# Optimization experiments

Measured on AMD Instinct MI355X. Metric: run time of the kernel, lower is better.

The kernel has to match this reference:

```python
import jax, jax.numpy as jnp
import numpy as np

B, N, D = 8, 2048, 512
S = 4096  # max_swaps


def setup_inputs() -> dict:
    key = jax.random.key(0)
    ks = jax.random.split(key, 5)
    h = jax.random.normal(ks[0], (B, N, D), dtype=jnp.float32)
    indices = jax.random.randint(ks[1], (B, S, 4), 0, N, dtype=jnp.int64)
    # MLP params (Linear stores weight as (out,in) in torch; we keep (in,out) and matmul)
    W1 = jax.random.normal(ks[2], (4 * D, D), dtype=jnp.float32) * (1.0 / np.sqrt(4 * D))
    b1 = jnp.zeros((D,), dtype=jnp.float32)
    W2 = jax.random.normal(ks[3], (D, D // 2), dtype=jnp.float32) * (1.0 / np.sqrt(D))
    b2 = jnp.zeros((D // 2,), dtype=jnp.float32)
    W3 = jax.random.normal(ks[4], (D // 2, 1), dtype=jnp.float32) * (1.0 / np.sqrt(D // 2))
    b3 = jnp.zeros((1,), dtype=jnp.float32)
    return {"h": h, "indices": indices, "W1": W1, "b1": b1, "W2": W2, "b2": b2, "W3": W3, "b3": b3}


def reference(h, indices, W1, b1, W2, b2, W3, b3):
    # h: (B, N, D); indices: (B, S, 4) node ids per swap
    swap_emb = jnp.take_along_axis(h[:, None, :, :], indices[..., None].astype(jnp.int32),
                                   axis=2)  # broadcast-gather -> (B, S, 4, D)
    # equivalently: h[batch_idx, indices]; implemented as per-batch gather
    swap_emb = jax.vmap(lambda hb, ib: hb[ib])(h, indices)  # (B, S, 4, D)
    swap_feats = swap_emb.reshape(h.shape[0], indices.shape[1], -1)  # (B, S, 4D)
    x = jax.nn.gelu(swap_feats @ W1 + b1, approximate=False)
    x = jax.nn.gelu(x @ W2 + b2, approximate=False)
    scores = (x @ W3 + b3)[..., 0]  # (B, S)
    rates = jax.nn.softplus(scores)
    return rates
```

## Files before the change

### kernel.cpp

```cpp
#include <hip/hip_runtime.h>
#include <math.h>

#define BATCH 8
#define NNODES 2048
#define DDIM 512
#define SWAPS 4096
#define M_TOTAL (BATCH * SWAPS)
#define MD (BATCH * NNODES)
#define KD DDIM
#define ND (4 * DDIM)
#define K2 DDIM
#define N2 (DDIM / 2)

typedef __attribute__((ext_vector_type(8))) __bf16 bf16x8;
typedef __attribute__((ext_vector_type(4))) float f32x4;
typedef __attribute__((ext_vector_type(8))) unsigned short us8;
typedef unsigned short ushort_t;

__device__ __forceinline__ float gelu_exact(float x) {
    return 0.5f * x * (1.0f + erff(x * 0.70710678118654752440f));
}
__device__ __forceinline__ float softplus_f(float x) {
    return fmaxf(x, 0.0f) + log1pf(expf(-fabsf(x)));
}
__device__ __forceinline__ unsigned short f2bf(float f) {
    unsigned int u = __builtin_bit_cast(unsigned int, f);
    u += 0x7FFFu + ((u >> 16) & 1u);
    return (unsigned short)(u >> 16);
}
__device__ __forceinline__ float bf2f(unsigned short s) {
    return __builtin_bit_cast(float, (unsigned int)s << 16);
}
__device__ __forceinline__ void glds16(const void* g, void* l) {
    __builtin_amdgcn_global_load_lds(
        (const __attribute__((address_space(1))) void*)g,
        (__attribute__((address_space(3))) void*)l, 16, 0, 0);
}

__global__ __launch_bounds__(256) void convert_kernel(
    const float* __restrict__ h, const float* __restrict__ W1,
    const float* __restrict__ W2, ushort_t* __restrict__ h_bf,
    ushort_t* __restrict__ W1pt, ushort_t* __restrict__ W2t)
{
    const int bid = blockIdx.x;
    if (bid < 8192) {
        size_t i = ((size_t)bid * 256 + threadIdx.x) * 4;
        float4 v = *(const float4*)(h + i);
        ushort4 o = { f2bf(v.x), f2bf(v.y), f2bf(v.z), f2bf(v.w) };
        *(ushort4*)(h_bf + i) = o;
    } else if (bid < 8192 + 1024) {
        size_t e = ((size_t)(bid - 8192) * 256 + threadIdx.x) * 4;
        const int k = (int)(e >> 9), n = (int)(e & 511);
        const int sg = k >> 9, d = k & 511;
        const int j = sg * 512 + n;
        float4 v = *(const float4*)(W1 + e);
        W1pt[(size_t)(j + 0) * KD + d] = f2bf(v.x);
        W1pt[(size_t)(j + 1) * KD + d] = f2bf(v.y);
        W1pt[(size_t)(j + 2) * KD + d] = f2bf(v.z);
        W1pt[(size_t)(j + 3) * KD + d] = f2bf(v.w);
    } else {
        size_t e = ((size_t)(bid - 9216) * 256 + threadIdx.x) * 4;
        const int k = (int)(e >> 8), n = (int)(e & 255);
        float4 v = *(const float4*)(W2 + e);
        W2t[(size_t)(n + 0) * K2 + k] = f2bf(v.x);
        W2t[(size_t)(n + 1) * K2 + k] = f2bf(v.y);
        W2t[(size_t)(n + 2) * K2 + k] = f2bf(v.z);
        W2t[(size_t)(n + 3) * K2 + k] = f2bf(v.w);
    }
}

__global__ __launch_bounds__(256) void gemm1_dense(
    const ushort_t* __restrict__ h_bf, const ushort_t* __restrict__ W1pt,
    ushort_t* __restrict__ P)
{
    __shared__ __align__(16) char smem[16384];

    const int tid = threadIdx.x;
    const int w = tid >> 6, lane = tid & 63;
    const int quad = lane >> 4, l16 = lane & 15;
    const int wr = w >> 1, wc = w & 1;

    const int bid = blockIdx.x;
    const int xcd = bid & 7;
    const int r = bid >> 3;
    const int m0 = xcd * NNODES + (r & 15) * 128;
    const int n0 = (r >> 4) * 128;

    const int row0 = tid >> 2, sub = tid & 3;
    const int cg = (sub - (row0 >> 1)) & 3;
    const ushort_t* bA0 = h_bf + (size_t)(m0 + row0) * KD + cg * 8;
    const ushort_t* bA1 = h_bf + (size_t)(m0 + row0 + 64) * KD + cg * 8;
    const ushort_t* bB0 = W1pt + (size_t)(n0 + row0) * KD + cg * 8;
    const ushort_t* bB1 = W1pt + (size_t)(n0 + row0 + 64) * KD + cg * 8;

    char* ldsA0 = smem + w * 1024;
    char* ldsA1 = smem + 4096 + w * 1024;
    char* ldsB0 = smem + 8192 + w * 1024;
    char* ldsB1 = smem + 12288 + w * 1024;

    int pa[4], pb[4];
    #pragma unroll
    for (int i = 0; i < 4; ++i) {
        const int rA = wr * 64 + i * 16 + l16;
        const int rB = wc * 64 + i * 16 + l16;
        pa[i] = rA * 64 + (((quad + (rA >> 1)) & 3) * 16);
        pb[i] = 8192 + rB * 64 + (((quad + (rB >> 1)) & 3) * 16);
    }

    f32x4 acc[4][4] = {};

    for (int kt = 0; kt < 16; ++kt) {
        const int oo = kt * 32;
        glds16(bA0 + oo, ldsA0);
        glds16(bA1 + oo, ldsA1);
        glds16(bB0 + oo, ldsB0);
        glds16(bB1 + oo, ldsB1);
        __syncthreads();
        bf16x8 af[4], bfr[4];
        #pragma unroll
        for (int i = 0; i < 4; ++i) {
            af[i]  = *(const bf16x8*)(smem + pa[i]);
            bfr[i] = *(const bf16x8*)(smem + pb[i]);
        }
        #pragma unroll
        for (int i = 0; i < 4; ++i)
            #pragma unroll
            for (int jj = 0; jj < 4; ++jj)
                acc[i][jj] = __builtin_amdgcn_mfma_f32_16x16x32_bf16(
                    af[i], bfr[jj], acc[i][jj], 0, 0, 0);
        __syncthreads();
    }

    #pragma unroll
    for (int jj = 0; jj < 4; ++jj) {
        const int n = n0 + wc * 64 + jj * 16 + l16;
        #pragma unroll
        for (int i = 0; i < 4; ++i) {
            f32x4 v = acc[i][jj];
            #pragma unroll
            for (int rr = 0; rr < 4; ++rr) {
                const int m = m0 + wr * 64 + i * 16 + quad * 4 + rr;
                P[(size_t)m * ND + n] = f2bf(v[rr]);
            }
        }
    }
}

__global__ __launch_bounds__(256) void gather_sum_kernel(
    const ushort_t* __restrict__ P, const int* __restrict__ idx,
    const float* __restrict__ b1, ushort_t* __restrict__ x1_bf)
{
    const int wave = threadIdx.x >> 6, lane = threadIdx.x & 63;
    const int m = blockIdx.x * 4 + wave;
    const int b = m >> 12;
    const int4 iv = *(const int4*)(idx + (size_t)m * 4);
    const ushort_t* Pb = P + (size_t)b * NNODES * ND;
    const int n = lane * 8;

    float s[8];
    {
        float4 ba = *(const float4*)(b1 + n);
        float4 bb = *(const float4*)(b1 + n + 4);
        s[0] = ba.x; s[1] = ba.y; s[2] = ba.z; s[3] = ba.w;
        s[4] = bb.x; s[5] = bb.y; s[6] = bb.z; s[7] = bb.w;
    }
    const int nodes[4] = { iv.x, iv.y, iv.z, iv.w };
    #pragma unroll
    for (int sg = 0; sg < 4; ++sg) {
        us8 v = *(const us8*)(Pb + (size_t)nodes[sg] * ND + sg * 512 + n);
        #pragma unroll
        for (int t = 0; t < 8; ++t) s[t] += bf2f(v[t]);
    }
    ushort4 o0 = { f2bf(gelu_exact(s[0])), f2bf(gelu_exact(s[1])),
                   f2bf(gelu_exact(s[2])), f2bf(gelu_exact(s[3])) };
    ushort4 o1 = { f2bf(gelu_exact(s[4])), f2bf(gelu_exact(s[5])),
                   f2bf(gelu_exact(s[6])), f2bf(gelu_exact(s[7])) };
    *(ushort4*)(x1_bf + (size_t)m * K2 + n) = o0;
    *(ushort4*)(x1_bf + (size_t)m * K2 + n + 4) = o1;
}

__global__ __launch_bounds__(256) void gemm2_partial(
    const ushort_t* __restrict__ x1_bf, const ushort_t* __restrict__ W2t,
    const float* __restrict__ b2, const float* __restrict__ W3,
    float* __restrict__ pp)
{
    __shared__ __align__(16) char smem[16384];

    const int tid = threadIdx.x;
    const int w = tid >> 6, lane = tid & 63;
    const int quad = lane >> 4, l16 = lane & 15;
    const int wr = w >> 1, wc = w & 1;
    const int m0 = blockIdx.y * 128, n0 = blockIdx.x * 128;

    const int row0 = tid >> 2, sub = tid & 3;
    const int cg = (sub - (row0 >> 1)) & 3;
    const ushort_t* bA0 = x1_bf + (size_t)(m0 + row0) * K2 + cg * 8;
    const ushort_t* bA1 = x1_bf + (size_t)(m0 + row0 + 64) * K2 + cg * 8;
    const ushort_t* bB0 = W2t + (size_t)(n0 + row0) * K2 + cg * 8;
    const ushort_t* bB1 = W2t + (size_t)(n0 + row0 + 64) * K2 + cg * 8;

    char* ldsA0 = smem + w * 1024;
    char* ldsA1 = smem + 4096 + w * 1024;
    char* ldsB0 = smem + 8192 + w * 1024;
    char* ldsB1 = smem + 12288 + w * 1024;

    int pa[4], pb[4];
    #pragma unroll
    for (int i = 0; i < 4; ++i) {
        const int rA = wr * 64 + i * 16 + l16;
        const int rB = wc * 64 + i * 16 + l16;
        pa[i] = rA * 64 + (((quad + (rA >> 1)) & 3) * 16);
        pb[i] = 8192 + rB * 64 + (((quad + (rB >> 1)) & 3) * 16);
    }

    f32x4 acc[4][4] = {};

    for (int kt = 0; kt < 16; ++kt) {
        const int oo = kt * 32;
        glds16(bA0 + oo, ldsA0);
        glds16(bA1 + oo, ldsA1);
        glds16(bB0 + oo, ldsB0);
        glds16(bB1 + oo, ldsB1);
        __syncthreads();
        bf16x8 af[4], bfr[4];
        #pragma unroll
        for (int i = 0; i < 4; ++i) {
            af[i]  = *(const bf16x8*)(smem + pa[i]);
            bfr[i] = *(const bf16x8*)(smem + pb[i]);
        }
        #pragma unroll
        for (int i = 0; i < 4; ++i)
            #pragma unroll
            for (int jj = 0; jj < 4; ++jj)
                acc[i][jj] = __builtin_amdgcn_mfma_f32_16x16x32_bf16(
                    af[i], bfr[jj], acc[i][jj], 0, 0, 0);
        __syncthreads();
    }

    float w3r[4], b2r[4];
    #pragma unroll
    for (int jj = 0; jj < 4; ++jj) {
        const int n = n0 + wc * 64 + jj * 16 + l16;
        w3r[jj] = W3[n];
        b2r[jj] = b2[n];
    }
    float part[4][4];
    #pragma unroll
    for (int i = 0; i < 4; ++i)
        #pragma unroll
        for (int rr = 0; rr < 4; ++rr) part[i][rr] = 0.0f;
    #pragma unroll
    for (int i = 0; i < 4; ++i)
        #pragma unroll
        for (int jj = 0; jj < 4; ++jj) {
            f32x4 v = acc[i][jj];
            #pragma unroll
            for (int rr = 0; rr < 4; ++rr)
                part[i][rr] = fmaf(gelu_exact(v[rr] + b2r[jj]), w3r[jj], part[i][rr]);
        }
    #pragma unroll
    for (int off = 1; off < 16; off <<= 1)
        #pragma unroll
        for (int i = 0; i < 4; ++i)
            #pragma unroll
            for (int rr = 0; rr < 4; ++rr)
                part[i][rr] += __shfl_xor(part[i][rr], off);

    float* red = (float*)smem;
    __syncthreads();
    if (wc == 1 && l16 == 0) {
        #pragma unroll
        for (int i = 0; i < 4; ++i)
            #pragma unroll
            for (int rr = 0; rr < 4; ++rr)
                red[wr * 64 + i * 16 + quad * 4 + rr] = part[i][rr];
    }
    __syncthreads();
    if (wc == 0 && l16 == 0) {
        float* dst = pp + (size_t)blockIdx.x * M_TOTAL + m0;
        #pragma unroll
        for (int i = 0; i < 4; ++i)
            #pragma unroll
            for (int rr = 0; rr < 4; ++rr) {
                const int r2 = wr * 64 + i * 16 + quad * 4 + rr;
                dst[r2] = part[i][rr] + red[r2];
            }
    }
}

__global__ __launch_bounds__(256) void finalize_head(
    const float* __restrict__ pp, const float* __restrict__ b3,
    float* __restrict__ out)
{
    const int m = blockIdx.x * 256 + threadIdx.x;
    out[m] = softplus_f(pp[m] + pp[M_TOTAL + m] + b3[0]);
}

extern "C" void kernel_launch(void* const* d_in, const int* in_sizes, int n_in,
                              void* d_out, int out_size, void* d_ws, size_t ws_size,
                              hipStream_t stream) {
    const float* h   = (const float*)d_in[0];
    const int*   idx = (const int*)d_in[1];
    const float* W1  = (const float*)d_in[2];
    const float* b1  = (const float*)d_in[3];
    const float* W2  = (const float*)d_in[4];
    const float* b2  = (const float*)d_in[5];
    const float* W3  = (const float*)d_in[6];
    const float* b3  = (const float*)d_in[7];
    float* out = (float*)d_out;

    char* ws = (char*)d_ws;
    ushort_t* P     = (ushort_t*)ws;
    float*    pp    = (float*)ws;
    ushort_t* h_bf  = (ushort_t*)(ws + (64u << 20));
    ushort_t* W1pt  = (ushort_t*)(ws + (80u << 20));
    ushort_t* x1_bf = (ushort_t*)(ws + (64u << 20));
    ushort_t* W2t   = (ushort_t*)(ws + (96u << 20));

    convert_kernel<<<9344, 256, 0, stream>>>(h, W1, W2, h_bf, W1pt, W2t);
    gemm1_dense<<<2048, 256, 0, stream>>>(h_bf, W1pt, P);
    gather_sum_kernel<<<M_TOTAL / 4, 256, 0, stream>>>(P, idx, b1, x1_bf);
    gemm2_partial<<<dim3(N2 / 128, M_TOTAL / 128), 256, 0, stream>>>(x1_bf, W2t, b2, W3, pp);
    finalize_head<<<M_TOTAL / 256, 256, 0, stream>>>(pp, b3, out);
}
```

Measured before the change: 203.9 us.

## Re-layout projected table by batch and column half; stage two K-tiles per barrier

```diff
diff --git a/kernel.cpp b/kernel.cpp
--- a/kernel.cpp
+++ b/kernel.cpp
@@ -6,7 +6,6 @@
 #define DDIM 512
 #define SWAPS 4096
 #define M_TOTAL (BATCH * SWAPS)
-#define MD (BATCH * NNODES)
 #define KD DDIM
 #define ND (4 * DDIM)
 #define K2 DDIM
@@ -71,9 +70,9 @@
 
 __global__ __launch_bounds__(256) void gemm1_dense(
     const ushort_t* __restrict__ h_bf, const ushort_t* __restrict__ W1pt,
-    ushort_t* __restrict__ P)
-{
-    __shared__ __align__(16) char smem[16384];
+    ushort_t* __restrict__ P2)
+{
+    __shared__ __align__(16) char smem[32768];
 
     const int tid = threadIdx.x;
     const int w = tid >> 6, lane = tid & 63;
@@ -93,11 +92,6 @@
     const ushort_t* bB0 = W1pt + (size_t)(n0 + row0) * KD + cg * 8;
     const ushort_t* bB1 = W1pt + (size_t)(n0 + row0 + 64) * KD + cg * 8;
 
-    char* ldsA0 = smem + w * 1024;
-    char* ldsA1 = smem + 4096 + w * 1024;
-    char* ldsB0 = smem + 8192 + w * 1024;
-    char* ldsB1 = smem + 12288 + w * 1024;
-
     int pa[4], pb[4];
     #pragma unroll
     for (int i = 0; i < 4; ++i) {
@@ -109,18 +103,21 @@
 
     f32x4 acc[4][4] = {};
 
-    for (int kt = 0; kt < 16; ++kt) {
+    auto stage = [&](int kt, int half) {
         const int oo = kt * 32;
-        glds16(bA0 + oo, ldsA0);
-        glds16(bA1 + oo, ldsA1);
-        glds16(bB0 + oo, ldsB0);
-        glds16(bB1 + oo, ldsB1);
-        __syncthreads();
+        char* base = smem + half * 16384;
+        glds16(bA0 + oo, base + w * 1024);
+        glds16(bA1 + oo, base + 4096 + w * 1024);
+        glds16(bB0 + oo, base + 8192 + w * 1024);
+        glds16(bB1 + oo, base + 12288 + w * 1024);
+    };
+    auto compute = [&](int half) {
+        const char* base = smem + half * 16384;
         bf16x8 af[4], bfr[4];
         #pragma unroll
         for (int i = 0; i < 4; ++i) {
-            af[i]  = *(const bf16x8*)(smem + pa[i]);
-            bfr[i] = *(const bf16x8*)(smem + pb[i]);
+            af[i]  = *(const bf16x8*)(base + pa[i]);
+            bfr[i] = *(const bf16x8*)(base + pb[i]);
         }
         #pragma unroll
         for (int i = 0; i < 4; ++i)
@@ -128,55 +125,71 @@
             for (int jj = 0; jj < 4; ++jj)
                 acc[i][jj] = __builtin_amdgcn_mfma_f32_16x16x32_bf16(
                     af[i], bfr[jj], acc[i][jj], 0, 0, 0);
+    };
+
+    for (int kt = 0; kt < 16; kt += 2) {
+        stage(kt, 0);
+        stage(kt + 1, 1);
         __syncthreads();
+        compute(0);
+        compute(1);
+        __syncthreads();
     }
 
     #pragma unroll
     for (int jj = 0; jj < 4; ++jj) {
-        const int n = n0 + wc * 64 + jj * 16 + l16;
+        const int j = n0 + wc * 64 + jj * 16 + l16;
+        const int sg = j >> 9, nh = j & 511;
+        const size_t base = ((size_t)(xcd * 2 + (nh >> 8)) * NNODES) * 1024
+                          + (size_t)(sg << 8) + (nh & 255);
         #pragma unroll
         for (int i = 0; i < 4; ++i) {
             f32x4 v = acc[i][jj];
             #pragma unroll
             for (int rr = 0; rr < 4; ++rr) {
-                const int m = m0 + wr * 64 + i * 16 + quad * 4 + rr;
-                P[(size_t)m * ND + n] = f2bf(v[rr]);
+                const int node = (m0 + wr * 64 + i * 16 + quad * 4 + rr) & (NNODES - 1);
+                P2[base + (size_t)node * 1024] = f2bf(v[rr]);
             }
         }
     }
 }
 
 __global__ __launch_bounds__(256) void gather_sum_kernel(
-    const ushort_t* __restrict__ P, const int* __restrict__ idx,
+    const ushort_t* __restrict__ P2, const int* __restrict__ idx,
     const float* __restrict__ b1, ushort_t* __restrict__ x1_bf)
 {
+    const int bid = blockIdx.x;
+    const int b = bid & 7;
+    const int t = bid >> 3;
+    const int nc = t >> 9;
+    const int rg = t & 511;
     const int wave = threadIdx.x >> 6, lane = threadIdx.x & 63;
-    const int m = blockIdx.x * 4 + wave;
-    const int b = m >> 12;
+    const int rsel = lane >> 5, li = lane & 31;
+    const int m = b * SWAPS + rg * 8 + wave * 2 + rsel;
     const int4 iv = *(const int4*)(idx + (size_t)m * 4);
-    const ushort_t* Pb = P + (size_t)b * NNODES * ND;
-    const int n = lane * 8;
+    const ushort_t* Pr = P2 + ((size_t)(b * 2 + nc) * NNODES) * 1024;
+    const int col = li * 8;
 
     float s[8];
     {
-        float4 ba = *(const float4*)(b1 + n);
-        float4 bb = *(const float4*)(b1 + n + 4);
+        const float* bp = b1 + nc * 256 + col;
+        float4 ba = *(const float4*)bp;
+        float4 bb = *(const float4*)(bp + 4);
         s[0] = ba.x; s[1] = ba.y; s[2] = ba.z; s[3] = ba.w;
         s[4] = bb.x; s[5] = bb.y; s[6] = bb.z; s[7] = bb.w;
     }
     const int nodes[4] = { iv.x, iv.y, iv.z, iv.w };
     #pragma unroll
     for (int sg = 0; sg < 4; ++sg) {
-        us8 v = *(const us8*)(Pb + (size_t)nodes[sg] * ND + sg * 512 + n);
-        #pragma unroll
-        for (int t = 0; t < 8; ++t) s[t] += bf2f(v[t]);
-    }
-    ushort4 o0 = { f2bf(gelu_exact(s[0])), f2bf(gelu_exact(s[1])),
-                   f2bf(gelu_exact(s[2])), f2bf(gelu_exact(s[3])) };
-    ushort4 o1 = { f2bf(gelu_exact(s[4])), f2bf(gelu_exact(s[5])),
-                   f2bf(gelu_exact(s[6])), f2bf(gelu_exact(s[7])) };
-    *(ushort4*)(x1_bf + (size_t)m * K2 + n) = o0;
-    *(ushort4*)(x1_bf + (size_t)m * K2 + n + 4) = o1;
+        us8 v = *(const us8*)(Pr + (size_t)nodes[sg] * 1024 + sg * 256 + col);
+        #pragma unroll
+        for (int u = 0; u < 8; ++u) s[u] += bf2f(v[u]);
+    }
+    us8 o;
+    #pragma unroll
+    for (int u = 0; u < 8; ++u)
+        o[u] = f2bf(gelu_exact(s[u]));
+    __builtin_nontemporal_store(o, (us8*)(x1_bf + (size_t)m * K2 + nc * 256 + col));
 }
 
 __global__ __launch_bounds__(256) void gemm2_partial(
@@ -184,7 +197,7 @@
     const float* __restrict__ b2, const float* __restrict__ W3,
     float* __restrict__ pp)
 {
-    __shared__ __align__(16) char smem[16384];
+    __shared__ __align__(16) char smem[32768];
 
     const int tid = threadIdx.x;
     const int w = tid >> 6, lane = tid & 63;
@@ -199,11 +212,6 @@
     const ushort_t* bB0 = W2t + (size_t)(n0 + row0) * K2 + cg * 8;
     const ushort_t* bB1 = W2t + (size_t)(n0 + row0 + 64) * K2 + cg * 8;
 
-    char* ldsA0 = smem + w * 1024;
-    char* ldsA1 = smem + 4096 + w * 1024;
-    char* ldsB0 = smem + 8192 + w * 1024;
-    char* ldsB1 = smem + 12288 + w * 1024;
-
     int pa[4], pb[4];
     #pragma unroll
     for (int i = 0; i < 4; ++i) {
@@ -215,18 +223,21 @@
 
     f32x4 acc[4][4] = {};
 
-    for (int kt = 0; kt < 16; ++kt) {
+    auto stage = [&](int kt, int half) {
         const int oo = kt * 32;
-        glds16(bA0 + oo, ldsA0);
-        glds16(bA1 + oo, ldsA1);
-        glds16(bB0 + oo, ldsB0);
-        glds16(bB1 + oo, ldsB1);
-        __syncthreads();
+        char* base = smem + half * 16384;
+        glds16(bA0 + oo, base + w * 1024);
+        glds16(bA1 + oo, base + 4096 + w * 1024);
+        glds16(bB0 + oo, base + 8192 + w * 1024);
+        glds16(bB1 + oo, base + 12288 + w * 1024);
+    };
+    auto compute = [&](int half) {
+        const char* base = smem + half * 16384;
         bf16x8 af[4], bfr[4];
         #pragma unroll
         for (int i = 0; i < 4; ++i) {
-            af[i]  = *(const bf16x8*)(smem + pa[i]);
-            bfr[i] = *(const bf16x8*)(smem + pb[i]);
+            af[i]  = *(const bf16x8*)(base + pa[i]);
+            bfr[i] = *(const bf16x8*)(base + pb[i]);
         }
         #pragma unroll
         for (int i = 0; i < 4; ++i)
@@ -234,6 +245,14 @@
             for (int jj = 0; jj < 4; ++jj)
                 acc[i][jj] = __builtin_amdgcn_mfma_f32_16x16x32_bf16(
                     af[i], bfr[jj], acc[i][jj], 0, 0, 0);
+    };
+
+    for (int kt = 0; kt < 16; kt += 2) {
+        stage(kt, 0);
+        stage(kt + 1, 1);
+        __syncthreads();
+        compute(0);
+        compute(1);
         __syncthreads();
     }
 
@@ -310,7 +329,7 @@
     float* out = (float*)d_out;
 
     char* ws = (char*)d_ws;
-    ushort_t* P     = (ushort_t*)ws;
+    ushort_t* P2    = (ushort_t*)ws;
     float*    pp    = (float*)ws;
     ushort_t* h_bf  = (ushort_t*)(ws + (64u << 20));
     ushort_t* W1pt  = (ushort_t*)(ws + (80u << 20));
@@ -318,8 +337,8 @@
     ushort_t* W2t   = (ushort_t*)(ws + (96u << 20));
 
     convert_kernel<<<9344, 256, 0, stream>>>(h, W1, W2, h_bf, W1pt, W2t);
-    gemm1_dense<<<2048, 256, 0, stream>>>(h_bf, W1pt, P);
-    gather_sum_kernel<<<M_TOTAL / 4, 256, 0, stream>>>(P, idx, b1, x1_bf);
+    gemm1_dense<<<2048, 256, 0, stream>>>(h_bf, W1pt, P2);
+    gather_sum_kernel<<<8192, 256, 0, stream>>>(P2, idx, b1, x1_bf);
     gemm2_partial<<<dim3(N2 / 128, M_TOTAL / 128), 256, 0, stream>>>(x1_bf, W2t, b2, W3, pp);
     finalize_head<<<M_TOTAL / 256, 256, 0, stream>>>(pp, b3, out);
 }
```

Result: no change. 202.6 us (-0.7%).
